# Kernel optimization log

Hardware: AMD Instinct MI355X
Metric: run time of the kernel (lower is better)

Reference implementation:

```python
import jax, jax.numpy as jnp
import numpy as np

H = 64  # hidden size

def setup_inputs() -> dict:
    key = jax.random.key(0)
    ks = jax.random.split(key, 7)
    B, T = 256, 5000
    s = 1.0 / np.sqrt(H)  # PyTorch LSTM init scale
    return {
        "x":    jax.random.normal(ks[0], (B, T), dtype=jnp.float32),
        "W_ih": jax.random.uniform(ks[1], (4 * H, 1), jnp.float32, -s, s),
        "W_hh": jax.random.uniform(ks[2], (4 * H, H), jnp.float32, -s, s),
        "b_ih": jax.random.uniform(ks[3], (4 * H,), jnp.float32, -s, s),
        "b_hh": jax.random.uniform(ks[4], (4 * H,), jnp.float32, -s, s),
        "W_fc": jax.random.uniform(ks[5], (128, H), jnp.float32, -s, s),
        "b_fc": jax.random.uniform(ks[6], (128,), jnp.float32, -s, s),
    }

def _lstm_last_hidden(x, W_ih, W_hh, b_ih, b_hh):
    # x: [B, T]; returns last hidden state h_T: [B, H]
    B, T = x.shape
    # input projection for all timesteps at once: [B, T, 4H]
    # (input_size == 1, so this is an outer product with W_ih[:, 0])
    x_proj = x[:, :, None] * W_ih[:, 0][None, None, :] + (b_ih + b_hh)

    def step(carry, xp_t):
        h, c = carry
        gates = xp_t + h @ W_hh.T  # [B, 4H]
        i = jax.nn.sigmoid(gates[:, 0 * H:1 * H])
        f = jax.nn.sigmoid(gates[:, 1 * H:2 * H])
        g = jnp.tanh(gates[:, 2 * H:3 * H])
        o = jax.nn.sigmoid(gates[:, 3 * H:4 * H])
        c = f * c + i * g
        h = o * jnp.tanh(c)
        return (h, c), None

    h0 = jnp.zeros((B, H), x.dtype)
    c0 = jnp.zeros((B, H), x.dtype)
    (h, c), _ = jax.lax.scan(step, (h0, c0), jnp.swapaxes(x_proj, 0, 1))
    return h

def reference(x, W_ih, W_hh, b_ih, b_hh, W_fc, b_fc):
    h_last = _lstm_last_hidden(x, W_ih, W_hh, b_ih, b_hh)  # [B, H]
    return jax.nn.relu(h_last @ W_fc.T + b_fc)  # [B, 128]
```

## Files before the change

kernel.cpp:

```cpp
#include <hip/hip_runtime.h>


#define LSTM_H 64
#define LSTM_T 5000
#define LSTM_B 256

typedef float v2f __attribute__((ext_vector_type(2)));

__device__ __forceinline__ void pk_fma_acc(v2f& acc, v2f a, v2f b) {
    asm("v_pk_fma_f32 %0, %1, %2, %0" : "+v"(acc) : "v"(a), "v"(b));
}

__device__ __forceinline__ float fast_rcp(float v) {
    return __builtin_amdgcn_rcpf(v);
}

__global__ __launch_bounds__(256) void ECGLSTM_lstm_fused(
    const float* __restrict__ x,
    const float* __restrict__ W_ih,
    const float* __restrict__ W_hh,
    const float* __restrict__ b_ih,
    const float* __restrict__ b_hh,
    const float* __restrict__ W_fc,
    const float* __restrict__ b_fc,
    float* __restrict__ out)
{
    const int tid  = threadIdx.x;
    const int lane = tid & 63;
    const int b    = blockIdx.x;

    __shared__ float xch[LSTM_T];
    __shared__ float hbuf[2][LSTM_H];
    __shared__ float gbuf[2][4 * LSTM_H];

    const float* xb = x + b * LSTM_T;
    for (int i = tid; i < LSTM_T; i += 256) xch[i] = xb[i];

    v2f w[LSTM_H / 2];
    {
        const float4* wrow = reinterpret_cast<const float4*>(W_hh + tid * LSTM_H);
        #pragma unroll
        for (int i = 0; i < LSTM_H / 4; ++i) {
            float4 v = wrow[i];
            w[2 * i]     = v2f{v.x, v.y};
            w[2 * i + 1] = v2f{v.z, v.w};
        }
    }
    const float wih  = W_ih[tid];
    const float bias = b_ih[tid] + b_hh[tid];
    const bool  is_tanh = ((tid >> 6) == 2);

    float c = 0.0f;
    hbuf[0][lane] = 0.0f;
    __syncthreads();

    #define LSTM_STEP(t, P)                                                    \
    {                                                                          \
        const float xv = xch[(t)];                          \
        v2f A = {0.f, 0.f}, C = {0.f, 0.f};                                    \
        const float4* h4 = reinterpret_cast<const float4*>(hbuf[(P)]);         \
        _Pragma("unroll")                                                      \
        for (int i = 0; i < LSTM_H / 4; ++i) {                                 \
            float4 hv = h4[i];                             \
            pk_fma_acc(A, v2f{hv.x, hv.y}, w[2 * i]);                          \
            pk_fma_acc(C, v2f{hv.z, hv.w}, w[2 * i + 1]);                      \
        }                                                                      \
        float g = fmaf(xv, wih, bias) + ((A.x + A.y) + (C.x + C.y));           \
        float act;                                                             \
        if (is_tanh) {                                                         \
            float e = __expf(2.0f * g);                                        \
            act = 1.0f - 2.0f * fast_rcp(e + 1.0f);                            \
        } else {                                                               \
            float e = __expf(-g);                                              \
            act = fast_rcp(1.0f + e);                                          \
        }                                                                      \
        gbuf[(P)][tid] = act;                                                  \
        __syncthreads();                                  \
        const float ig = gbuf[(P)][lane];                                      \
        const float fg = gbuf[(P)][LSTM_H + lane];                             \
        const float gg = gbuf[(P)][2 * LSTM_H + lane];                         \
        const float og = gbuf[(P)][3 * LSTM_H + lane];                         \
        c = fmaf(fg, c, ig * gg);                                              \
        float e2 = __expf(2.0f * c);                                           \
        float th = 1.0f - 2.0f * fast_rcp(e2 + 1.0f);                          \
        hbuf[1 - (P)][lane] = og * th;                    \
    }

    for (int t = 0; t < LSTM_T; t += 2) {
        LSTM_STEP(t, 0);
        LSTM_STEP(t + 1, 1);
    }
    #undef LSTM_STEP

    if (tid < 128) {
        float s = b_fc[tid];
        const float4* wf = reinterpret_cast<const float4*>(W_fc + tid * LSTM_H);
        const float4* h4 = reinterpret_cast<const float4*>(hbuf[0]);
        #pragma unroll
        for (int i = 0; i < LSTM_H / 4; ++i) {
            float4 wv = wf[i];
            float4 hv = h4[i];
            s = fmaf(hv.x, wv.x, s);
            s = fmaf(hv.y, wv.y, s);
            s = fmaf(hv.z, wv.z, s);
            s = fmaf(hv.w, wv.w, s);
        }
        out[b * 128 + tid] = fmaxf(s, 0.0f);
    }
}

extern "C" void kernel_launch(void* const* d_in, const int* in_sizes, int n_in,
                              void* d_out, int out_size, void* d_ws, size_t ws_size,
                              hipStream_t stream) {
    const float* x    = (const float*)d_in[0];
    const float* W_ih = (const float*)d_in[1];
    const float* W_hh = (const float*)d_in[2];
    const float* b_ih = (const float*)d_in[3];
    const float* b_hh = (const float*)d_in[4];
    const float* W_fc = (const float*)d_in[5];
    const float* b_fc = (const float*)d_in[6];
    float* out = (float*)d_out;

    ECGLSTM_lstm_fused<<<LSTM_B, 256, 0, stream>>>(
        x, W_ih, W_hh, b_ih, b_hh, W_fc, b_fc, out);
}
```

Before: 2.075 ms.

## Run each sequence on a single wavefront computing all four gates per lane

Each block now runs one 64-lane wavefront instead of four. Every lane holds the recurrent weight rows for all four gates of its hidden unit and computes i, f, g and o itself. This removes the shared gate buffer and the per-step __syncthreads exchange, and relies on in-wave LDS ordering for the hidden-state handoff. The cost is four times the serial FMA work per lane, about 256 weight VGPRs per lane, and only one SIMD active per block.

```diff
diff --git a/kernel.cpp b/kernel.cpp
--- a/kernel.cpp
+++ b/kernel.cpp
@@ -15,7 +15,7 @@
     return __builtin_amdgcn_rcpf(v);
 }
 
-__global__ __launch_bounds__(256) void ECGLSTM_lstm_fused(
+__global__ __launch_bounds__(64, 1) void ECGLSTM_lstm_1wave(
     const float* __restrict__ x,
     const float* __restrict__ W_ih,
     const float* __restrict__ W_hh,
@@ -25,65 +25,72 @@
     const float* __restrict__ b_fc,
     float* __restrict__ out)
 {
-    const int tid  = threadIdx.x;
-    const int lane = tid & 63;
-    const int b    = blockIdx.x;
+    const int u = threadIdx.x;
+    const int b = blockIdx.x;
 
     __shared__ float xch[LSTM_T];
     __shared__ float hbuf[2][LSTM_H];
-    __shared__ float gbuf[2][4 * LSTM_H];
 
     const float* xb = x + b * LSTM_T;
-    for (int i = tid; i < LSTM_T; i += 256) xch[i] = xb[i];
+    for (int i = u; i < LSTM_T; i += 64) xch[i] = xb[i];
 
-    v2f w[LSTM_H / 2];
+    v2f wi[LSTM_H / 2], wf[LSTM_H / 2], wg[LSTM_H / 2], wo[LSTM_H / 2];
     {
-        const float4* wrow = reinterpret_cast<const float4*>(W_hh + tid * LSTM_H);
+        const float4* ri = reinterpret_cast<const float4*>(W_hh + (0 * LSTM_H + u) * LSTM_H);
+        const float4* rf = reinterpret_cast<const float4*>(W_hh + (1 * LSTM_H + u) * LSTM_H);
+        const float4* rg = reinterpret_cast<const float4*>(W_hh + (2 * LSTM_H + u) * LSTM_H);
+        const float4* ro = reinterpret_cast<const float4*>(W_hh + (3 * LSTM_H + u) * LSTM_H);
         #pragma unroll
         for (int i = 0; i < LSTM_H / 4; ++i) {
-            float4 v = wrow[i];
-            w[2 * i]     = v2f{v.x, v.y};
-            w[2 * i + 1] = v2f{v.z, v.w};
+            float4 vi = ri[i], vf = rf[i], vg = rg[i], vo = ro[i];
+            wi[2 * i] = v2f{vi.x, vi.y}; wi[2 * i + 1] = v2f{vi.z, vi.w};
+            wf[2 * i] = v2f{vf.x, vf.y}; wf[2 * i + 1] = v2f{vf.z, vf.w};
+            wg[2 * i] = v2f{vg.x, vg.y}; wg[2 * i + 1] = v2f{vg.z, vg.w};
+            wo[2 * i] = v2f{vo.x, vo.y}; wo[2 * i + 1] = v2f{vo.z, vo.w};
         }
     }
-    const float wih  = W_ih[tid];
-    const float bias = b_ih[tid] + b_hh[tid];
-    const bool  is_tanh = ((tid >> 6) == 2);
+    const float wih_i = W_ih[0 * LSTM_H + u];
+    const float wih_f = W_ih[1 * LSTM_H + u];
+    const float wih_g = W_ih[2 * LSTM_H + u];
+    const float wih_o = W_ih[3 * LSTM_H + u];
+    const float bias_i = b_ih[0 * LSTM_H + u] + b_hh[0 * LSTM_H + u];
+    const float bias_f = b_ih[1 * LSTM_H + u] + b_hh[1 * LSTM_H + u];
+    const float bias_g = b_ih[2 * LSTM_H + u] + b_hh[2 * LSTM_H + u];
+    const float bias_o = b_ih[3 * LSTM_H + u] + b_hh[3 * LSTM_H + u];
 
     float c = 0.0f;
-    hbuf[0][lane] = 0.0f;
-    __syncthreads();
+    hbuf[0][u] = 0.0f;
 
     #define LSTM_STEP(t, P)                                                    \
     {                                                                          \
         const float xv = xch[(t)];                          \
-        v2f A = {0.f, 0.f}, C = {0.f, 0.f};                                    \
+        v2f Ai = {0.f,0.f}, Ci = {0.f,0.f};                                    \
+        v2f Af = {0.f,0.f}, Cf = {0.f,0.f};                                    \
+        v2f Ag = {0.f,0.f}, Cg = {0.f,0.f};                                    \
+        v2f Ao = {0.f,0.f}, Co = {0.f,0.f};                                    \
         const float4* h4 = reinterpret_cast<const float4*>(hbuf[(P)]);         \
         _Pragma("unroll")                                                      \
         for (int i = 0; i < LSTM_H / 4; ++i) {                                 \
             float4 hv = h4[i];                             \
-            pk_fma_acc(A, v2f{hv.x, hv.y}, w[2 * i]);                          \
-            pk_fma_acc(C, v2f{hv.z, hv.w}, w[2 * i + 1]);                      \
+            v2f hlo = v2f{hv.x, hv.y};                                         \
+            v2f hhi = v2f{hv.z, hv.w};                                         \
+            pk_fma_acc(Ai, hlo, wi[2 * i]); pk_fma_acc(Ci, hhi, wi[2 * i + 1]);\
+            pk_fma_acc(Af, hlo, wf[2 * i]); pk_fma_acc(Cf, hhi, wf[2 * i + 1]);\
+            pk_fma_acc(Ag, hlo, wg[2 * i]); pk_fma_acc(Cg, hhi, wg[2 * i + 1]);\
+            pk_fma_acc(Ao, hlo, wo[2 * i]); pk_fma_acc(Co, hhi, wo[2 * i + 1]);\
         }                                                                      \
-        float g = fmaf(xv, wih, bias) + ((A.x + A.y) + (C.x + C.y));           \
-        float act;                                                             \
-        if (is_tanh) {                                                         \
-            float e = __expf(2.0f * g);                                        \
-            act = 1.0f - 2.0f * fast_rcp(e + 1.0f);                            \
-        } else {                                                               \
-            float e = __expf(-g);                                              \
-            act = fast_rcp(1.0f + e);                                          \
-        }                                                                      \
-        gbuf[(P)][tid] = act;                                                  \
-        __syncthreads();                                  \
-        const float ig = gbuf[(P)][lane];                                      \
-        const float fg = gbuf[(P)][LSTM_H + lane];                             \
-        const float gg = gbuf[(P)][2 * LSTM_H + lane];                         \
-        const float og = gbuf[(P)][3 * LSTM_H + lane];                         \
-        c = fmaf(fg, c, ig * gg);                                              \
+        float gi = fmaf(xv, wih_i, bias_i) + ((Ai.x + Ai.y) + (Ci.x + Ci.y));  \
+        float gf = fmaf(xv, wih_f, bias_f) + ((Af.x + Af.y) + (Cf.x + Cf.y));  \
+        float gg = fmaf(xv, wih_g, bias_g) + ((Ag.x + Ag.y) + (Cg.x + Cg.y));  \
+        float go = fmaf(xv, wih_o, bias_o) + ((Ao.x + Ao.y) + (Co.x + Co.y));  \
+        float ei = __expf(-gi);        float i_ = fast_rcp(1.0f + ei);         \
+        float ef = __expf(-gf);        float f_ = fast_rcp(1.0f + ef);         \
+        float eg = __expf(2.0f * gg);  float g_ = 1.0f - 2.0f * fast_rcp(eg + 1.0f); \
+        float eo = __expf(-go);        float o_ = fast_rcp(1.0f + eo);         \
+        c = fmaf(f_, c, i_ * g_);                                              \
         float e2 = __expf(2.0f * c);                                           \
         float th = 1.0f - 2.0f * fast_rcp(e2 + 1.0f);                          \
-        hbuf[1 - (P)][lane] = og * th;                    \
+        hbuf[1 - (P)][u] = o_ * th;                                            \
     }
 
     for (int t = 0; t < LSTM_T; t += 2) {
@@ -92,20 +99,27 @@
     }
     #undef LSTM_STEP
 
-    if (tid < 128) {
-        float s = b_fc[tid];
-        const float4* wf = reinterpret_cast<const float4*>(W_fc + tid * LSTM_H);
+    float4 hreg[LSTM_H / 4];
+    {
         const float4* h4 = reinterpret_cast<const float4*>(hbuf[0]);
         #pragma unroll
+        for (int i = 0; i < LSTM_H / 4; ++i) hreg[i] = h4[i];
+    }
+    #pragma unroll
+    for (int r0 = 0; r0 < 2; ++r0) {
+        const int r = u + r0 * 64;
+        float s = b_fc[r];
+        const float4* wf4 = reinterpret_cast<const float4*>(W_fc + r * LSTM_H);
+        #pragma unroll
         for (int i = 0; i < LSTM_H / 4; ++i) {
-            float4 wv = wf[i];
-            float4 hv = h4[i];
+            float4 wv = wf4[i];
+            float4 hv = hreg[i];
             s = fmaf(hv.x, wv.x, s);
             s = fmaf(hv.y, wv.y, s);
             s = fmaf(hv.z, wv.z, s);
             s = fmaf(hv.w, wv.w, s);
         }
-        out[b * 128 + tid] = fmaxf(s, 0.0f);
+        out[b * 128 + r] = fmaxf(s, 0.0f);
     }
 }
 
@@ -121,6 +135,6 @@
     const float* b_fc = (const float*)d_in[6];
     float* out = (float*)d_out;
 
-    ECGLSTM_lstm_fused<<<LSTM_B, 256, 0, stream>>>(
+    ECGLSTM_lstm_1wave<<<LSTM_B, 64, 0, stream>>>(
         x, W_ih, W_hh, b_ih, b_hh, W_fc, b_fc, out);
 }
```

After: 5.763 ms. +177.8%, slower.

## Interleave LSTM gates per quad and exchange activations via DPP broadcasts

Applied to the files above, without the earlier changes.

Threads are remapped so that each group of four adjacent lanes holds the i, f, g and o gate rows for one hidden unit. DPP quad broadcasts then share the four activations inside the register file, replacing the shared-memory gate buffer and its round trip. The per-step barrier moves to after the h write, one lane per quad stores h, and a branch-free activation formula replaces the tanh/sigmoid branch. The dot product now uses four accumulators for more instruction-level parallelism. The aim is to cut LDS traffic and latency on the serial per-timestep critical path.

```diff
diff --git a/kernel.cpp b/kernel.cpp
--- a/kernel.cpp
+++ b/kernel.cpp
@@ -15,7 +15,15 @@
     return __builtin_amdgcn_rcpf(v);
 }
 
-__global__ __launch_bounds__(256) void ECGLSTM_lstm_fused(
+template<int K>
+__device__ __forceinline__ float quad_bcast(float v) {
+    constexpr int ctrl = K | (K << 2) | (K << 4) | (K << 6);
+    int r = __builtin_amdgcn_mov_dpp(__builtin_bit_cast(int, v),
+                                     ctrl, 0xf, 0xf, false);
+    return __builtin_bit_cast(float, r);
+}
+
+__global__ __launch_bounds__(256) void ECGLSTM_lstm_quad(
     const float* __restrict__ x,
     const float* __restrict__ W_ih,
     const float* __restrict__ W_hh,
@@ -27,63 +35,68 @@
 {
     const int tid  = threadIdx.x;
     const int lane = tid & 63;
+    const int w    = tid >> 6;
+    const int g    = lane & 3;
+    const int ul   = lane >> 2;
+    const int u    = w * 16 + ul;
     const int b    = blockIdx.x;
 
     __shared__ float xch[LSTM_T];
     __shared__ float hbuf[2][LSTM_H];
-    __shared__ float gbuf[2][4 * LSTM_H];
 
     const float* xb = x + b * LSTM_T;
     for (int i = tid; i < LSTM_T; i += 256) xch[i] = xb[i];
 
-    v2f w[LSTM_H / 2];
+    const int row = g * LSTM_H + u;
+    v2f wreg[LSTM_H / 2];
     {
-        const float4* wrow = reinterpret_cast<const float4*>(W_hh + tid * LSTM_H);
+        const float4* wrow = reinterpret_cast<const float4*>(W_hh + row * LSTM_H);
         #pragma unroll
         for (int i = 0; i < LSTM_H / 4; ++i) {
             float4 v = wrow[i];
-            w[2 * i]     = v2f{v.x, v.y};
-            w[2 * i + 1] = v2f{v.z, v.w};
+            wreg[2 * i]     = v2f{v.x, v.y};
+            wreg[2 * i + 1] = v2f{v.z, v.w};
         }
     }
-    const float wih  = W_ih[tid];
-    const float bias = b_ih[tid] + b_hh[tid];
-    const bool  is_tanh = ((tid >> 6) == 2);
+    const float wih  = W_ih[row];
+    const float bias = b_ih[row] + b_hh[row];
+    const bool  is_t = (g == 2);
+    const float aexp = is_t ? -2.0f : -1.0f;
+    const float smul = is_t ?  2.0f :  1.0f;
+    const float dadd = is_t ? -1.0f :  0.0f;
 
     float c = 0.0f;
-    hbuf[0][lane] = 0.0f;
+    if (tid < LSTM_H) hbuf[0][tid] = 0.0f;
     __syncthreads();
 
     #define LSTM_STEP(t, P)                                                    \
     {                                                                          \
         const float xv = xch[(t)];                          \
-        v2f A = {0.f, 0.f}, C = {0.f, 0.f};                                    \
+        v2f a0 = {0.f,0.f}, a1 = {0.f,0.f}, a2 = {0.f,0.f}, a3 = {0.f,0.f};    \
         const float4* h4 = reinterpret_cast<const float4*>(hbuf[(P)]);         \
         _Pragma("unroll")                                                      \
-        for (int i = 0; i < LSTM_H / 4; ++i) {                                 \
-            float4 hv = h4[i];                             \
-            pk_fma_acc(A, v2f{hv.x, hv.y}, w[2 * i]);                          \
-            pk_fma_acc(C, v2f{hv.z, hv.w}, w[2 * i + 1]);                      \
+        for (int i = 0; i < LSTM_H / 4; i += 2) {                              \
+            float4 hva = h4[i];                            \
+            float4 hvb = h4[i + 1];                                            \
+            pk_fma_acc(a0, v2f{hva.x, hva.y}, wreg[2 * i]);                    \
+            pk_fma_acc(a1, v2f{hva.z, hva.w}, wreg[2 * i + 1]);                \
+            pk_fma_acc(a2, v2f{hvb.x, hvb.y}, wreg[2 * i + 2]);                \
+            pk_fma_acc(a3, v2f{hvb.z, hvb.w}, wreg[2 * i + 3]);                \
         }                                                                      \
-        float g = fmaf(xv, wih, bias) + ((A.x + A.y) + (C.x + C.y));           \
-        float act;                                                             \
-        if (is_tanh) {                                                         \
-            float e = __expf(2.0f * g);                                        \
-            act = 1.0f - 2.0f * fast_rcp(e + 1.0f);                            \
-        } else {                                                               \
-            float e = __expf(-g);                                              \
-            act = fast_rcp(1.0f + e);                                          \
-        }                                                                      \
-        gbuf[(P)][tid] = act;                                                  \
-        __syncthreads();                                  \
-        const float ig = gbuf[(P)][lane];                                      \
-        const float fg = gbuf[(P)][LSTM_H + lane];                             \
-        const float gg = gbuf[(P)][2 * LSTM_H + lane];                         \
-        const float og = gbuf[(P)][3 * LSTM_H + lane];                         \
-        c = fmaf(fg, c, ig * gg);                                              \
+        float dot = ((a0.x + a0.y) + (a1.x + a1.y))                            \
+                  + ((a2.x + a2.y) + (a3.x + a3.y));                           \
+        float gv  = fmaf(xv, wih, bias) + dot;                                 \
+        float e   = __expf(aexp * gv);                                         \
+        float act = fmaf(smul, fast_rcp(1.0f + e), dadd);                      \
+        float i_  = quad_bcast<0>(act);                                        \
+        float f_  = quad_bcast<1>(act);                                        \
+        float g_  = quad_bcast<2>(act);                                        \
+        float o_  = quad_bcast<3>(act);                                        \
+        c = fmaf(f_, c, i_ * g_);                                              \
         float e2 = __expf(2.0f * c);                                           \
         float th = 1.0f - 2.0f * fast_rcp(e2 + 1.0f);                          \
-        hbuf[1 - (P)][lane] = og * th;                    \
+        if (g == 0) hbuf[1 - (P)][u] = o_ * th;             \
+        __syncthreads();                                  \
     }
 
     for (int t = 0; t < LSTM_T; t += 2) {
@@ -121,6 +134,6 @@
     const float* b_fc = (const float*)d_in[6];
     float* out = (float*)d_out;
 
-    ECGLSTM_lstm_fused<<<LSTM_B, 256, 0, stream>>>(
+    ECGLSTM_lstm_quad<<<LSTM_B, 256, 0, stream>>>(
         x, W_ih, W_hh, b_ih, b_hh, W_fc, b_fc, out);
 }
```

New measurement: 1.999 ms. 3.7% less time.

## Broadcast hidden state via readlane instead of LDS round-trip

Applied to the files above, without the earlier changes.

Each lane now keeps its own hidden element in a register, and the recurrent matvec broadcasts h across the wavefront with v_readlane. This replaces writing h to shared memory and reading it back as float4, so one LDS store/load stage leaves each timestep's critical path. The sigmoid/tanh branch is also merged into a single branch-free formula driven by per-wave constants. The cost is 64 readlanes plus scalar-operand FMAs instead of packed FMAs, which may add instruction count and SALU-to-VALU dependency stalls.

```diff
diff --git a/kernel.cpp b/kernel.cpp
--- a/kernel.cpp
+++ b/kernel.cpp
@@ -5,17 +5,16 @@
 #define LSTM_T 5000
 #define LSTM_B 256
 
-typedef float v2f __attribute__((ext_vector_type(2)));
-
-__device__ __forceinline__ void pk_fma_acc(v2f& acc, v2f a, v2f b) {
-    asm("v_pk_fma_f32 %0, %1, %2, %0" : "+v"(acc) : "v"(a), "v"(b));
-}
-
 __device__ __forceinline__ float fast_rcp(float v) {
     return __builtin_amdgcn_rcpf(v);
 }
 
-__global__ __launch_bounds__(256) void ECGLSTM_lstm_fused(
+__device__ __forceinline__ float lane_bcast(float v, int k) {
+    return __builtin_bit_cast(float,
+        __builtin_amdgcn_readlane(__builtin_bit_cast(int, v), k));
+}
+
+__global__ __launch_bounds__(256) void ECGLSTM_lstm_rl(
     const float* __restrict__ x,
     const float* __restrict__ W_ih,
     const float* __restrict__ W_hh,
@@ -27,63 +26,64 @@
 {
     const int tid  = threadIdx.x;
     const int lane = tid & 63;
+    const int w    = tid >> 6;
     const int b    = blockIdx.x;
 
     __shared__ float xch[LSTM_T];
-    __shared__ float hbuf[2][LSTM_H];
-    __shared__ float gbuf[2][4 * LSTM_H];
+    __shared__ float gbuf[2][4][LSTM_H];
+    __shared__ float hfin[LSTM_H];
 
     const float* xb = x + b * LSTM_T;
     for (int i = tid; i < LSTM_T; i += 256) xch[i] = xb[i];
 
-    v2f w[LSTM_H / 2];
+    float wreg[LSTM_H];
     {
         const float4* wrow = reinterpret_cast<const float4*>(W_hh + tid * LSTM_H);
         #pragma unroll
         for (int i = 0; i < LSTM_H / 4; ++i) {
             float4 v = wrow[i];
-            w[2 * i]     = v2f{v.x, v.y};
-            w[2 * i + 1] = v2f{v.z, v.w};
+            wreg[4 * i]     = v.x;
+            wreg[4 * i + 1] = v.y;
+            wreg[4 * i + 2] = v.z;
+            wreg[4 * i + 3] = v.w;
         }
     }
     const float wih  = W_ih[tid];
     const float bias = b_ih[tid] + b_hh[tid];
-    const bool  is_tanh = ((tid >> 6) == 2);
+    const bool  is_t = (w == 2);
+    const float aexp = is_t ? -2.0f : -1.0f;
+    const float smul = is_t ?  2.0f :  1.0f;
+    const float dadd = is_t ? -1.0f :  0.0f;
 
-    float c = 0.0f;
-    hbuf[0][lane] = 0.0f;
+    float hv = 0.0f;
+    float c  = 0.0f;
     __syncthreads();
 
     #define LSTM_STEP(t, P)                                                    \
     {                                                                          \
         const float xv = xch[(t)];                          \
-        v2f A = {0.f, 0.f}, C = {0.f, 0.f};                                    \
-        const float4* h4 = reinterpret_cast<const float4*>(hbuf[(P)]);         \
+        float a0 = 0.f, a1 = 0.f, a2 = 0.f, a3 = 0.f;                          \
         _Pragma("unroll")                                                      \
-        for (int i = 0; i < LSTM_H / 4; ++i) {                                 \
-            float4 hv = h4[i];                             \
-            pk_fma_acc(A, v2f{hv.x, hv.y}, w[2 * i]);                          \
-            pk_fma_acc(C, v2f{hv.z, hv.w}, w[2 * i + 1]);                      \
+        for (int j = 0; j < 16; ++j) {                                         \
+            a0 = fmaf(lane_bcast(hv, j),      wreg[j],      a0);               \
+            a1 = fmaf(lane_bcast(hv, j + 16), wreg[j + 16], a1);               \
+            a2 = fmaf(lane_bcast(hv, j + 32), wreg[j + 32], a2);               \
+            a3 = fmaf(lane_bcast(hv, j + 48), wreg[j + 48], a3);               \
         }                                                                      \
-        float g = fmaf(xv, wih, bias) + ((A.x + A.y) + (C.x + C.y));           \
-        float act;                                                             \
-        if (is_tanh) {                                                         \
-            float e = __expf(2.0f * g);                                        \
-            act = 1.0f - 2.0f * fast_rcp(e + 1.0f);                            \
-        } else {                                                               \
-            float e = __expf(-g);                                              \
-            act = fast_rcp(1.0f + e);                                          \
-        }                                                                      \
-        gbuf[(P)][tid] = act;                                                  \
+        float dot = (a0 + a1) + (a2 + a3);                                     \
+        float gv  = fmaf(xv, wih, bias) + dot;                                 \
+        float e   = __expf(aexp * gv);                                         \
+        float act = fmaf(smul, fast_rcp(1.0f + e), dadd);                      \
+        gbuf[(P)][w][lane] = act;                           \
         __syncthreads();                                  \
-        const float ig = gbuf[(P)][lane];                                      \
-        const float fg = gbuf[(P)][LSTM_H + lane];                             \
-        const float gg = gbuf[(P)][2 * LSTM_H + lane];                         \
-        const float og = gbuf[(P)][3 * LSTM_H + lane];                         \
+        const float ig = gbuf[(P)][0][lane];                                   \
+        const float fg = gbuf[(P)][1][lane];                                   \
+        const float gg = gbuf[(P)][2][lane];                                   \
+        const float og = gbuf[(P)][3][lane];                                   \
         c = fmaf(fg, c, ig * gg);                                              \
         float e2 = __expf(2.0f * c);                                           \
         float th = 1.0f - 2.0f * fast_rcp(e2 + 1.0f);                          \
-        hbuf[1 - (P)][lane] = og * th;                    \
+        hv = og * th;                                    \
     }
 
     for (int t = 0; t < LSTM_T; t += 2) {
@@ -92,18 +92,20 @@
     }
     #undef LSTM_STEP
 
+    if (tid < LSTM_H) hfin[tid] = hv;
+    __syncthreads();
     if (tid < 128) {
         float s = b_fc[tid];
         const float4* wf = reinterpret_cast<const float4*>(W_fc + tid * LSTM_H);
-        const float4* h4 = reinterpret_cast<const float4*>(hbuf[0]);
+        const float4* h4 = reinterpret_cast<const float4*>(hfin);
         #pragma unroll
         for (int i = 0; i < LSTM_H / 4; ++i) {
             float4 wv = wf[i];
-            float4 hv = h4[i];
-            s = fmaf(hv.x, wv.x, s);
-            s = fmaf(hv.y, wv.y, s);
-            s = fmaf(hv.z, wv.z, s);
-            s = fmaf(hv.w, wv.w, s);
+            float4 hvv = h4[i];
+            s = fmaf(hvv.x, wv.x, s);
+            s = fmaf(hvv.y, wv.y, s);
+            s = fmaf(hvv.z, wv.z, s);
+            s = fmaf(hvv.w, wv.w, s);
         }
         out[b * 128 + tid] = fmaxf(s, 0.0f);
     }
@@ -121,6 +123,6 @@
     const float* b_fc = (const float*)d_in[6];
     float* out = (float*)d_out;
 
-    ECGLSTM_lstm_fused<<<LSTM_B, 256, 0, stream>>>(
+    ECGLSTM_lstm_rl<<<LSTM_B, 256, 0, stream>>>(
         x, W_ih, W_hh, b_ih, b_hh, W_fc, b_fc, out);
 }
```

After: 2.130 ms. +2.7%, slower.
